# Optimization experiments

Hardware: AMD Instinct MI355X
Metric: run time of the kernel (lower is better)

Reference implementation:

```python
import jax, jax.numpy as jnp
import numpy as np

K = 20      # self.k in OurModel
TAU = 1.0   # self.tau in OurModel


def _knn_feats(emb, idx, yctx):
    # emb: [N, E] embedding table; idx: [B] int query ids; yctx: [B, N] residual context
    a = emb[idx]                                            # [B, E] gathered query embeddings
    # squared euclidean via gram trick, then sqrt == torch.cdist(p=2)
    d2 = (jnp.sum(a * a, axis=-1, keepdims=True)
          + jnp.sum(emb * emb, axis=-1)[None, :]
          - 2.0 * a @ emb.T)                                 # [B, N]
    sim = jnp.sqrt(jnp.clip(d2, 0.0, None)) + 0.001
    rows = jnp.arange(idx.shape[0])
    sim = sim.at[rows, idx].set(0.0)                         # zero self-distance
    w = jnp.exp(-sim / TAU)                                  # [B, N], self weight == 1 (max)
    # top (K+1) weights; drop the largest (the self entry) -> top-K neighbours.
    # Matches torch argsort(w)[:, -(K+1):-1]; downstream ops are order-invariant reductions.
    topw, topi = jax.lax.top_k(w, K + 1)
    topw = topw[:, 1:]                                       # [B, K]
    sel = jnp.take_along_axis(yctx, topi[:, 1:], axis=1)     # [B, K]
    f1 = jnp.sum(topw, axis=1)                               # sum of weights
    f2 = jnp.sum(sel * topw, axis=1) / jnp.sum(topw, axis=1) # weighted mean
    f3 = jnp.std(sel, axis=1, ddof=1)                        # torch.std is unbiased
    return f1, f2, f3


def _forward(emb0, emb1, rctx0, rctx1, idx0, idx1, mean_in, std_in,
             W1, b1, Wm, bm, Ws, bs):
    a1, a2, a3 = _knn_feats(emb0, idx0, rctx0)
    b1_, b2_, b3_ = _knn_feats(emb1, idx1, rctx1)
    # torch.cat(final1 + final2 + final3 + [mean, std]) column order
    feats = jnp.stack([a1, b1_, a2, b2_, a3, b3_, mean_in, std_in], axis=1)  # [B, 8]
    h = jnp.maximum(feats @ W1 + b1, 0.0)                    # [B, 64]
    mean_out = h @ Wm + bm[0]                                # [B]
    std_out = h @ Ws + bs[0]                                 # [B]
    return mean_out, std_out


def setup_inputs() -> dict:
    key = jax.random.key(0)
    ks = jax.random.split(key, 14)
    B, N, E, H = 512, 50000, 16, 64
    return {
        "emb0": jax.random.normal(ks[0], (N, E), jnp.float32),
        "emb1": jax.random.normal(ks[1], (N, E), jnp.float32),
        "rctx0": jax.random.normal(ks[2], (B, N), jnp.float32),
        "rctx1": jax.random.normal(ks[3], (B, N), jnp.float32),
        "idx0": jax.random.randint(ks[4], (B,), 0, N, jnp.int32),
        "idx1": jax.random.randint(ks[5], (B,), 0, N, jnp.int32),
        "mean_in": jax.random.normal(ks[6], (B,), jnp.float32),
        "std_in": jax.random.normal(ks[7], (B,), jnp.float32),
        "W1": jax.random.normal(ks[8], (8, H), jnp.float32) * 0.1,
        "b1": jax.random.normal(ks[9], (H,), jnp.float32) * 0.1,
        "Wm": jax.random.normal(ks[10], (H,), jnp.float32) * 0.1,
        "bm": jax.random.normal(ks[11], (1,), jnp.float32) * 0.1,
        "Ws": jax.random.normal(ks[12], (H,), jnp.float32) * 0.1,
        "bs": jax.random.normal(ks[13], (1,), jnp.float32) * 0.1,
    }


def reference(emb0, emb1, rctx0, rctx1, idx0, idx1, mean_in, std_in,
              W1, b1, Wm, bm, Ws, bs):
    return _forward(emb0, emb1, rctx0, rctx1, idx0, idx1, mean_in, std_in,
                    W1, b1, Wm, bm, Ws, bs)
```

## Files before the change

### kernel.cpp

```cpp
#include <hip/hip_runtime.h>
#include <math.h>

typedef unsigned long long u64;
typedef unsigned int u32;
#define INF64 0xFFFFFFFFFFFFFFFFULL
#define FBIG 3.3e38f
#define KSEL 20
#define QT   32
#define CNK  32
#define CNKSH 5
#define CAP  256
#define PREFT 2
#define DEPS 0.5f
#define NTHR 512

typedef __bf16 bf16x8 __attribute__((ext_vector_type(8)));
typedef float  f32x16 __attribute__((ext_vector_type(16)));
typedef unsigned int uint4e __attribute__((ext_vector_type(4)));

static __device__ __forceinline__ u32 asu(float f) { return __builtin_bit_cast(u32, f); }
static __device__ __forceinline__ float trunchi(u32 u) { return __builtin_bit_cast(float, u & 0xffff0000u); }
#define PERM2(a,b) __builtin_amdgcn_perm((a),(b),0x07060302u)
static __device__ __forceinline__ bf16x8 mk8(u32 a, u32 b, u32 c, u32 d) {
    uint4e t = {a, b, c, d};
    return __builtin_bit_cast(bf16x8, t);
}
static __device__ __forceinline__ f32x16 zero16() {
    f32x16 z = {0.f,0.f,0.f,0.f,0.f,0.f,0.f,0.f,0.f,0.f,0.f,0.f,0.f,0.f,0.f,0.f};
    return z;
}

static __device__ __forceinline__ float dot16(
    float4 a0, float4 a1, float4 a2, float4 a3,
    float4 b0, float4 b1, float4 b2, float4 b3)
{
    float d = 0.f;
    d = fmaf(a0.x, b0.x, d); d = fmaf(a0.y, b0.y, d);
    d = fmaf(a0.z, b0.z, d); d = fmaf(a0.w, b0.w, d);
    d = fmaf(a1.x, b1.x, d); d = fmaf(a1.y, b1.y, d);
    d = fmaf(a1.z, b1.z, d); d = fmaf(a1.w, b1.w, d);
    d = fmaf(a2.x, b2.x, d); d = fmaf(a2.y, b2.y, d);
    d = fmaf(a2.z, b2.z, d); d = fmaf(a2.w, b2.w, d);
    d = fmaf(a3.x, b3.x, d); d = fmaf(a3.y, b3.y, d);
    d = fmaf(a3.z, b3.z, d); d = fmaf(a3.w, b3.w, d);
    return d;
}

static __device__ __forceinline__ void cvt_hilo(float4 f0, float4 f1, bf16x8& hi, bf16x8& lo) {
    u32 u0=asu(f0.x),u1=asu(f0.y),u2=asu(f0.z),u3=asu(f0.w);
    u32 u4=asu(f1.x),u5=asu(f1.y),u6=asu(f1.z),u7=asu(f1.w);
    hi = mk8(PERM2(u1,u0), PERM2(u3,u2), PERM2(u5,u4), PERM2(u7,u6));
    u32 w0=asu(f0.x-trunchi(u0)), w1=asu(f0.y-trunchi(u1));
    u32 w2=asu(f0.z-trunchi(u2)), w3=asu(f0.w-trunchi(u3));
    u32 w4=asu(f1.x-trunchi(u4)), w5=asu(f1.y-trunchi(u5));
    u32 w6=asu(f1.z-trunchi(u6)), w7=asu(f1.w-trunchi(u7));
    lo = mk8(PERM2(w1,w0), PERM2(w3,w2), PERM2(w5,w4), PERM2(w7,w6));
}

static __device__ __forceinline__ f32x16 tile_qe(
    const float* __restrict__ embS, int base, int col, int kb, int N,
    bf16x8 B1, bf16x8 B2)
{
    int row = base + col;
    row = min(row, N - 1);
    const float4* ep = (const float4*)(embS + (size_t)row * 16 + kb * 8);
    float4 f0 = ep[0], f1 = ep[1];
    bf16x8 A1, A2;
    cvt_hilo(f0, f1, A1, A2);
    f32x16 acc = zero16();
    acc = __builtin_amdgcn_mfma_f32_32x32x16_bf16(A1, B1, acc, 0, 0, 0);
    acc = __builtin_amdgcn_mfma_f32_32x32x16_bf16(A1, B2, acc, 0, 0, 0);
    acc = __builtin_amdgcn_mfma_f32_32x32x16_bf16(A2, B1, acc, 0, 0, 0);
    return acc;
}

__global__ __launch_bounds__(256) void norm_kernel(
    const float* __restrict__ emb0, const float* __restrict__ emb1,
    float* __restrict__ neBuf, int N, int npad)
{
    const int j = blockIdx.x * 256 + threadIdx.x;
    const float* __restrict__ e = blockIdx.y ? emb1 : emb0;
    float* __restrict__ o = neBuf + (size_t)blockIdx.y * npad;
    float v = FBIG;
    if (j < N) {
        const float4* p = (const float4*)(e + (size_t)j * 16);
        float4 e0=p[0],e1=p[1],e2=p[2],e3=p[3];
        v = dot16(e0,e1,e2,e3, e0,e1,e2,e3);
    }
    if (j < npad) o[j] = v;
}

__device__ __attribute__((noinline)) float bound21(const float* sMinq, int lane) {
    const u32 vb = (lane < 32) ? asu(sMinq[lane]) : 0xFFFFFFFFu;
    u32 T = 0;
#pragma unroll 1
    for (int bb = 30; bb >= 16; --bb) {
        u32 U = T | ((1u << bb) - 1u);
        int nle = __popcll(__ballot(vb <= U));
        if (nle < KSEL + 1) T |= (1u << bb);
    }
    return __uint_as_float(T | 0xFFFFu) + DEPS;
}

__device__ __attribute__((noinline)) void refine_q(
    const float* __restrict__ embS, const float* __restrict__ neS,
    const u32* __restrict__ sbufq, const float4* qp, float naq,
    int M, u64* __restrict__ dst, int lane)
{
    const float4 q0 = qp[0], q1 = qp[1], q2 = qp[2], q3 = qp[3];
    auto rk = [&](int i) -> u64 {
        int j = (int)sbufq[i];
        const float4* p = (const float4*)(embS + (size_t)j * 16);
        float4 e0 = p[0], e1 = p[1], e2 = p[2], e3 = p[3];
        float qe = dot16(q0, q1, q2, q3, e0, e1, e2, e3);
        float dd = fmaxf(fmaf(qe, -2.f, naq + neS[j]), 0.f);
        return ((u64)asu(dd) << 32) | (u32)j;
    };
    u64 k0 = (lane < M) ? rk(lane) : INF64;
    if (M <= 64) {
        u64 T = 0;
#pragma unroll 1
        for (int bb = 62; bb >= 32; --bb) {
            u64 U = T | ((1ull << bb) - 1ull);
            int nle = __popcll(__ballot(k0 <= U));
            if (nle < KSEL) T |= (1ull << bb);
        }
        {
            u64 U = T | 0xFFFFull;
            int m = __popcll(__ballot(k0 <= U));
            if (m == KSEL) T = U;
            else {
#pragma unroll 1
                for (int bb = 15; bb >= 0; --bb) {
                    u64 U2 = T | ((1ull << bb) - 1ull);
                    int nle = __popcll(__ballot(k0 <= U2));
                    if (nle < KSEL) T |= (1ull << bb);
                }
            }
        }
        u64 mm = __ballot(k0 <= T);
        if (k0 <= T) {
            int sl = __popcll(mm & ((1ull << lane) - 1ull));
            if (sl < KSEL) dst[sl] = k0;
        }
        for (int sl = __popcll(mm) + lane; sl < KSEL; sl += 64) dst[sl] = INF64;
    } else {
        u64 k1 = (lane + 64 < M)  ? rk(lane + 64)  : INF64;
        u64 k2 = (lane + 128 < M) ? rk(lane + 128) : INF64;
        u64 k3 = (lane + 192 < M) ? rk(lane + 192) : INF64;
        u64 T = 0;
#pragma unroll 1
        for (int bb = 62; bb >= 32; --bb) {
            u64 U = T | ((1ull << bb) - 1ull);
            int nle = __popcll(__ballot(k0 <= U)) + __popcll(__ballot(k1 <= U))
                    + __popcll(__ballot(k2 <= U)) + __popcll(__ballot(k3 <= U));
            if (nle < KSEL) T |= (1ull << bb);
        }
        {
            u64 U = T | 0xFFFFull;
            int m = __popcll(__ballot(k0 <= U)) + __popcll(__ballot(k1 <= U))
                  + __popcll(__ballot(k2 <= U)) + __popcll(__ballot(k3 <= U));
            if (m == KSEL) T = U;
            else {
#pragma unroll 1
                for (int bb = 15; bb >= 0; --bb) {
                    u64 U2 = T | ((1ull << bb) - 1ull);
                    int nle = __popcll(__ballot(k0 <= U2)) + __popcll(__ballot(k1 <= U2))
                            + __popcll(__ballot(k2 <= U2)) + __popcll(__ballot(k3 <= U2));
                    if (nle < KSEL) T |= (1ull << bb);
                }
            }
        }
        int basec = 0;
        {
            u64 mm = __ballot(k0 <= T);
            if (k0 <= T) { int sl = basec + __popcll(mm & ((1ull << lane) - 1ull)); if (sl < KSEL) dst[sl] = k0; }
            basec += __popcll(mm);
        }
        {
            u64 mm = __ballot(k1 <= T);
            if (k1 <= T) { int sl = basec + __popcll(mm & ((1ull << lane) - 1ull)); if (sl < KSEL) dst[sl] = k1; }
            basec += __popcll(mm);
        }
        {
            u64 mm = __ballot(k2 <= T);
            if (k2 <= T) { int sl = basec + __popcll(mm & ((1ull << lane) - 1ull)); if (sl < KSEL) dst[sl] = k2; }
            basec += __popcll(mm);
        }
        {
            u64 mm = __ballot(k3 <= T);
            if (k3 <= T) { int sl = basec + __popcll(mm & ((1ull << lane) - 1ull)); if (sl < KSEL) dst[sl] = k3; }
            basec += __popcll(mm);
        }
        for (int sl = basec + lane; sl < KSEL; sl += 64) dst[sl] = INF64;
    }
}

__global__ __launch_bounds__(NTHR, 8) void knn_scan_kernel(
    const float* __restrict__ emb0, const float* __restrict__ emb1,
    const int* __restrict__ idx0, const int* __restrict__ idx1,
    const float* __restrict__ neBuf,
    u64* __restrict__ chunkTop, int N, int B, int chlen)
{
    const int tid  = threadIdx.x;
    const int lane = tid & 63;
    const int wv   = tid >> 6;
    const int col  = lane & 31;
    const int kb   = lane >> 5;
    const int bx   = blockIdx.x;
    const int xcd  = bx & 7;
    const int s    = xcd & 1;
    const int t_   = (bx >> 3) * 4 + (xcd >> 1);
    const int c    = t_ & (CNK - 1);
    const int qt   = t_ >> CNKSH;
    const int qbase = qt * QT;
    const int jbeg = c * chlen;
    const int tpc  = chlen >> 5;
    const int npad = chlen * CNK;

    const float* __restrict__ embS = s ? emb1 : emb0;
    const int*   __restrict__ idxp = s ? idx1 : idx0;
    const float* __restrict__ neS  = neBuf + (size_t)s * npad;

    __shared__ float Qs[QT][16];
    __shared__ float naS[QT];
    __shared__ int   sq[QT];
    __shared__ int   scnt[QT];
    __shared__ float sthr[QT];
    __shared__ float sMin[QT][33];
    __shared__ u32   sbuf[QT][CAP];

    if (tid < QT) { sq[tid] = idxp[qbase + tid]; scnt[tid] = 0; }
    __syncthreads();
    if (tid < 128) {
        int q = tid >> 2, part = tid & 3;
        ((float4*)(&Qs[q][0]))[part] = ((const float4*)(embS + (size_t)sq[q] * 16))[part];
    }
    __syncthreads();
    if (tid < QT) {
        const float4* qp = (const float4*)(&Qs[tid][0]);
        float4 a0=qp[0],a1=qp[1],a2=qp[2],a3=qp[3];
        naS[tid] = dot16(a0,a1,a2,a3, a0,a1,a2,a3);
    }
    bf16x8 B1, B2;
    {
        const float4* qp = (const float4*)(&Qs[col][kb * 8]);
        float4 f0 = qp[0], f1 = qp[1];
        cvt_hilo(f0, f1, B1, B2);
    }
    __syncthreads();

    const float na_l  = naS[col];
    const int   self_l = sq[col];

    float m0v = FBIG, m1v = FBIG;
#define PINS(r, nef) { float v_ = fmaf(acc[r], -2.f, na_l + (nef)); \
    float t1_ = fminf(m1v, fmaxf(m0v, v_)); m0v = fminf(m0v, v_); m1v = t1_; }
    for (int pt = 0; pt < PREFT; ++pt) {
        const int t = wv + pt * 8;
        const int base = jbeg + t * 32;
        const float4* np_ = (const float4*)(neS + base + kb * 4);
        float4 n0 = np_[0], n1 = np_[2], n2 = np_[4], n3 = np_[6];
        f32x16 acc = tile_qe(embS, base, col, kb, N, B1, B2);
        PINS(0,n0.x)  PINS(1,n0.y)  PINS(2,n0.z)  PINS(3,n0.w)
        PINS(4,n1.x)  PINS(5,n1.y)  PINS(6,n1.z)  PINS(7,n1.w)
        PINS(8,n2.x)  PINS(9,n2.y)  PINS(10,n2.z) PINS(11,n2.w)
        PINS(12,n3.x) PINS(13,n3.y) PINS(14,n3.z) PINS(15,n3.w)
    }
#undef PINS
    sMin[col][(wv * 2 + kb) * 2 + 0] = fmaxf(m0v, 0.f);
    sMin[col][(wv * 2 + kb) * 2 + 1] = fmaxf(m1v, 0.f);
    __syncthreads();

    for (int qq = 0; qq < 4; ++qq) {
        const int q = wv * 4 + qq;
        float thr = bound21(&sMin[q][0], lane);
        if (lane == 0) sthr[q] = thr;
    }
    __syncthreads();
    const float thr_l = sthr[col];

#define EPI(r, nef) { float ad_ = fmaf(acc[r], -2.f, na_l + (nef)); \
    if (ad_ <= thr_l) msk |= (1u << (r)); }
    for (int t = wv; t < tpc; t += 8) {
        const int base = jbeg + t * 32;
        const float4* np_ = (const float4*)(neS + base + kb * 4);
        float4 n0 = np_[0], n1 = np_[2], n2 = np_[4], n3 = np_[6];
        f32x16 acc = tile_qe(embS, base, col, kb, N, B1, B2);
        u32 msk = 0;
        EPI(0,n0.x)  EPI(1,n0.y)  EPI(2,n0.z)  EPI(3,n0.w)
        EPI(4,n1.x)  EPI(5,n1.y)  EPI(6,n1.z)  EPI(7,n1.w)
        EPI(8,n2.x)  EPI(9,n2.y)  EPI(10,n2.z) EPI(11,n2.w)
        EPI(12,n3.x) EPI(13,n3.y) EPI(14,n3.z) EPI(15,n3.w)
        while (msk) {
            int r = __ffs(msk) - 1;
            msk &= msk - 1;
            int j = base + (r & 3) + 8 * (r >> 2) + 4 * kb;
            if (j != self_l) {
                int sl = atomicAdd(&scnt[col], 1);
                if (sl < CAP) sbuf[col][sl] = (u32)j;
            }
        }
    }
#undef EPI
    __syncthreads();

    for (int qq = 0; qq < 4; ++qq) {
        const int q = wv * 4 + qq;
        u64* dst = chunkTop + ((size_t)(s * B + qbase + q) * CNK + c) * KSEL;
        refine_q(embS, neS, &sbuf[q][0], (const float4*)(&Qs[q][0]), naS[q],
                 min(scnt[q], CAP), dst, lane);
    }
}

__global__ __launch_bounds__(128) void merge_mlp_kernel(
    const u64* __restrict__ chunkTop,
    const float* __restrict__ rctx0, const float* __restrict__ rctx1,
    const float* __restrict__ mean_in, const float* __restrict__ std_in,
    const float* __restrict__ W1, const float* __restrict__ b1,
    const float* __restrict__ Wm, const float* __restrict__ bm,
    const float* __restrict__ Ws, const float* __restrict__ bs,
    float* __restrict__ out, int N, int B)
{
    const int b = blockIdx.x;
    const int tid = threadIdx.x;
    const int s = tid >> 6;
    const int lane = tid & 63;
    __shared__ float sf[8];

    const u64* src = chunkTop + ((size_t)(s * B + b)) * (CNK * KSEL);
    u64 v0 = src[lane];
    u64 v1 = src[lane + 64];
    u64 v2 = src[lane + 128];
    u64 v3 = src[lane + 192];
    u64 v4 = src[lane + 256];
    u64 v5 = src[lane + 320];
    u64 v6 = src[lane + 384];
    u64 v7 = src[lane + 448];
    u64 v8 = src[lane + 512];
    u64 v9 = src[lane + 576];
#define NLE(U) (__popcll(__ballot(v0 <= (U))) + __popcll(__ballot(v1 <= (U))) \
              + __popcll(__ballot(v2 <= (U))) + __popcll(__ballot(v3 <= (U))) \
              + __popcll(__ballot(v4 <= (U))) + __popcll(__ballot(v5 <= (U))) \
              + __popcll(__ballot(v6 <= (U))) + __popcll(__ballot(v7 <= (U))) \
              + __popcll(__ballot(v8 <= (U))) + __popcll(__ballot(v9 <= (U))))
    u64 T = 0;
#pragma unroll 1
    for (int bb = 62; bb >= 32; --bb) {
        u64 U = T | ((1ull << bb) - 1ull);
        int nle = NLE(U);
        if (nle < KSEL) T |= (1ull << bb);
    }
    {
        u64 U = T | 0xFFFFull;
        int m = NLE(U);
        if (m == KSEL) T = U;
        else {
#pragma unroll 1
            for (int bb = 15; bb >= 0; --bb) {
                u64 U2 = T | ((1ull << bb) - 1ull);
                int nle = NLE(U2);
                if (nle < KSEL) T |= (1ull << bb);
            }
        }
    }
#undef NLE
    const float* __restrict__ rctx = s ? rctx1 : rctx0;
    float sw = 0.f, ssw = 0.f, ss = 0.f, ss2 = 0.f;
#define ACC(vx) if ((vx) <= T) { \
        float d2 = __uint_as_float((u32)((vx) >> 32)); \
        int j = (int)(u32)((vx) & 0xFFFFFFFFULL); \
        float sim = sqrtf(d2) + 0.001f; \
        float wr = expf(-sim); \
        float svr = rctx[(size_t)b * N + j]; \
        sw += wr; ssw += svr * wr; ss += svr; ss2 += svr * svr; }
    ACC(v0) ACC(v1) ACC(v2) ACC(v3) ACC(v4)
    ACC(v5) ACC(v6) ACC(v7) ACC(v8) ACC(v9)
#undef ACC
#pragma unroll
    for (int o = 32; o; o >>= 1) {
        sw  += __shfl_down(sw,  o, 64);
        ssw += __shfl_down(ssw, o, 64);
        ss  += __shfl_down(ss,  o, 64);
        ss2 += __shfl_down(ss2, o, 64);
    }
    if (lane == 0) {
        sf[0 + s] = sw;
        sf[2 + s] = ssw / sw;
        float mean = ss * (1.f / KSEL);
        float var = (ss2 - (float)KSEL * mean * mean) * (1.f / (KSEL - 1));
        sf[4 + s] = sqrtf(fmaxf(var, 0.f));
        if (s == 0) { sf[6] = mean_in[b]; sf[7] = std_in[b]; }
    }
    __syncthreads();

    if (tid < 64) {
        float f0 = sf[0], f1 = sf[1], f2 = sf[2], f3 = sf[3];
        float f4 = sf[4], f5 = sf[5], f6 = sf[6], f7 = sf[7];
        float h = b1[lane];
        h = fmaf(f0, W1[0 * 64 + lane], h);
        h = fmaf(f1, W1[1 * 64 + lane], h);
        h = fmaf(f2, W1[2 * 64 + lane], h);
        h = fmaf(f3, W1[3 * 64 + lane], h);
        h = fmaf(f4, W1[4 * 64 + lane], h);
        h = fmaf(f5, W1[5 * 64 + lane], h);
        h = fmaf(f6, W1[6 * 64 + lane], h);
        h = fmaf(f7, W1[7 * 64 + lane], h);
        h = fmaxf(h, 0.f);
        float mo = h * Wm[lane], so = h * Ws[lane];
#pragma unroll
        for (int o = 32; o; o >>= 1) {
            mo += __shfl_down(mo, o, 64);
            so += __shfl_down(so, o, 64);
        }
        if (lane == 0) {
            out[b] = mo + bm[0];
            out[B + b] = so + bs[0];
        }
    }
}

extern "C" void kernel_launch(void* const* d_in, const int* in_sizes, int n_in,
                              void* d_out, int out_size, void* d_ws, size_t ws_size,
                              hipStream_t stream) {
    const float* emb0    = (const float*)d_in[0];
    const float* emb1    = (const float*)d_in[1];
    const float* rctx0   = (const float*)d_in[2];
    const float* rctx1   = (const float*)d_in[3];
    const int*   idx0    = (const int*)d_in[4];
    const int*   idx1    = (const int*)d_in[5];
    const float* mean_in = (const float*)d_in[6];
    const float* std_in  = (const float*)d_in[7];
    const float* W1      = (const float*)d_in[8];
    const float* b1      = (const float*)d_in[9];
    const float* Wm      = (const float*)d_in[10];
    const float* bm      = (const float*)d_in[11];
    const float* Ws      = (const float*)d_in[12];
    const float* bs      = (const float*)d_in[13];

    const int B = in_sizes[4];
    const int N = in_sizes[0] / 16;

    int chlen = (((N + CNK - 1) / CNK) + 31) & ~31;
    int npad  = chlen * CNK;

    float* neBuf = (float*)d_ws;
    u64* chunkTop = (u64*)((char*)d_ws + (size_t)2 * npad * sizeof(float));

    norm_kernel<<<dim3(npad / 256, 2), 256, 0, stream>>>(emb0, emb1, neBuf, N, npad);

    knn_scan_kernel<<<dim3(2 * (B / QT) * CNK), NTHR, 0, stream>>>(
        emb0, emb1, idx0, idx1, neBuf, chunkTop, N, B, chlen);

    merge_mlp_kernel<<<dim3(B), 128, 0, stream>>>(
        chunkTop, rctx0, rctx1, mean_in, std_in,
        W1, b1, Wm, bm, Ws, bs, (float*)d_out, N, B);
}
```

Measured before the change: 281.6 us.

## Prepack bf16 hi/lo embeddings, fold norms into MFMA accumulator, quantize refine selection

A prep kernel now converts each embedding row once into packed bf16 hi/lo halves alongside the squared norms. The scan kernel loads these packed words directly instead of converting per tile. It also seeds the MFMA accumulator with -0.5*(|q|^2+|e|^2), so the epilogue becomes a single compare against a scaled threshold. The refine step ranks candidates by a 16-bit quantized distance key, falls back to full 64-bit keys only for ties, and the prefetch tile count is doubled. The cost is extra workspace and memory traffic for the packed copy, plus an extra tie-resolution path.

After: 289.0 us. 2.6% more time.

```diff
diff --git a/kernel.cpp b/kernel.cpp
--- a/kernel.cpp
+++ b/kernel.cpp
@@ -10,7 +10,7 @@
 #define CNK  32
 #define CNKSH 5
 #define CAP  256
-#define PREFT 2
+#define PREFT 4
 #define DEPS 0.5f
 #define NTHR 512
 
@@ -24,10 +24,6 @@
 static __device__ __forceinline__ bf16x8 mk8(u32 a, u32 b, u32 c, u32 d) {
     uint4e t = {a, b, c, d};
     return __builtin_bit_cast(bf16x8, t);
-}
-static __device__ __forceinline__ f32x16 zero16() {
-    f32x16 z = {0.f,0.f,0.f,0.f,0.f,0.f,0.f,0.f,0.f,0.f,0.f,0.f,0.f,0.f,0.f,0.f};
-    return z;
 }
 
 static __device__ __forceinline__ float dot16(
@@ -58,36 +54,46 @@
 }
 
 static __device__ __forceinline__ f32x16 tile_qe(
-    const float* __restrict__ embS, int base, int col, int kb, int N,
-    bf16x8 B1, bf16x8 B2)
+    const u32* __restrict__ packS, int base, int col, int kb, int N,
+    bf16x8 B1, bf16x8 B2, f32x16 acc)
 {
     int row = base + col;
     row = min(row, N - 1);
-    const float4* ep = (const float4*)(embS + (size_t)row * 16 + kb * 8);
-    float4 f0 = ep[0], f1 = ep[1];
-    bf16x8 A1, A2;
-    cvt_hilo(f0, f1, A1, A2);
-    f32x16 acc = zero16();
+    const uint4e* ph = (const uint4e*)(packS + (size_t)row * 16);
+    bf16x8 A1 = __builtin_bit_cast(bf16x8, ph[kb]);
+    bf16x8 A2 = __builtin_bit_cast(bf16x8, ph[2 + kb]);
     acc = __builtin_amdgcn_mfma_f32_32x32x16_bf16(A1, B1, acc, 0, 0, 0);
     acc = __builtin_amdgcn_mfma_f32_32x32x16_bf16(A1, B2, acc, 0, 0, 0);
     acc = __builtin_amdgcn_mfma_f32_32x32x16_bf16(A2, B1, acc, 0, 0, 0);
     return acc;
 }
 
-__global__ __launch_bounds__(256) void norm_kernel(
+__global__ __launch_bounds__(256) void prep_kernel(
     const float* __restrict__ emb0, const float* __restrict__ emb1,
-    float* __restrict__ neBuf, int N, int npad)
+    float* __restrict__ neBuf, u32* __restrict__ pack, int N, int npad)
 {
     const int j = blockIdx.x * 256 + threadIdx.x;
+    if (j >= npad) return;
     const float* __restrict__ e = blockIdx.y ? emb1 : emb0;
     float* __restrict__ o = neBuf + (size_t)blockIdx.y * npad;
+    uint4e* __restrict__ pk = (uint4e*)(pack + ((size_t)blockIdx.y * npad + j) * 16);
     float v = FBIG;
+    uint4e z = {0u, 0u, 0u, 0u};
+    uint4e s0 = z, s1 = z, s2 = z, s3 = z;
     if (j < N) {
         const float4* p = (const float4*)(e + (size_t)j * 16);
         float4 e0=p[0],e1=p[1],e2=p[2],e3=p[3];
         v = dot16(e0,e1,e2,e3, e0,e1,e2,e3);
-    }
-    if (j < npad) o[j] = v;
+        bf16x8 h0, l0, h1, l1;
+        cvt_hilo(e0, e1, h0, l0);
+        cvt_hilo(e2, e3, h1, l1);
+        s0 = __builtin_bit_cast(uint4e, h0);
+        s1 = __builtin_bit_cast(uint4e, h1);
+        s2 = __builtin_bit_cast(uint4e, l0);
+        s3 = __builtin_bit_cast(uint4e, l1);
+    }
+    o[j] = v;
+    pk[0] = s0; pk[1] = s1; pk[2] = s2; pk[3] = s3;
 }
 
 __device__ __attribute__((noinline)) float bound21(const float* sMinq, int lane) {
@@ -104,92 +110,109 @@
 
 __device__ __attribute__((noinline)) void refine_q(
     const float* __restrict__ embS, const float* __restrict__ neS,
-    const u32* __restrict__ sbufq, const float4* qp, float naq,
+    const u32* __restrict__ sbufq, const float4* qp, float naq, float thrq,
     int M, u64* __restrict__ dst, int lane)
 {
     const float4 q0 = qp[0], q1 = qp[1], q2 = qp[2], q3 = qp[3];
-    auto rk = [&](int i) -> u64 {
+    const float qsc = 65536.0f / (thrq + 0.25f);
+    auto rk = [&](int i, u32& di) -> u64 {
         int j = (int)sbufq[i];
         const float4* p = (const float4*)(embS + (size_t)j * 16);
         float4 e0 = p[0], e1 = p[1], e2 = p[2], e3 = p[3];
         float qe = dot16(q0, q1, q2, q3, e0, e1, e2, e3);
         float dd = fmaxf(fmaf(qe, -2.f, naq + neS[j]), 0.f);
+        di = min((u32)(dd * qsc), 0xFFFFu);
         return ((u64)asu(dd) << 32) | (u32)j;
     };
-    u64 k0 = (lane < M) ? rk(lane) : INF64;
     if (M <= 64) {
-        u64 T = 0;
-#pragma unroll 1
-        for (int bb = 62; bb >= 32; --bb) {
-            u64 U = T | ((1ull << bb) - 1ull);
-            int nle = __popcll(__ballot(k0 <= U));
-            if (nle < KSEL) T |= (1ull << bb);
-        }
-        {
-            u64 U = T | 0xFFFFull;
-            int m = __popcll(__ballot(k0 <= U));
-            if (m == KSEL) T = U;
-            else {
-#pragma unroll 1
-                for (int bb = 15; bb >= 0; --bb) {
-                    u64 U2 = T | ((1ull << bb) - 1ull);
-                    int nle = __popcll(__ballot(k0 <= U2));
-                    if (nle < KSEL) T |= (1ull << bb);
-                }
+        u32 d0 = 0xFFFFFFFFu; u64 k0 = INF64;
+        if (lane < M) k0 = rk(lane, d0);
+        u32 T = 0;
+#pragma unroll 1
+        for (int bb = 15; bb >= 0; --bb) {
+            u32 U = T | ((1u << bb) - 1u);
+            int nle = __popcll(__ballot(d0 <= U));
+            if (nle < KSEL) T |= (1u << bb);
+        }
+        int c1 = __popcll(__ballot(d0 < T));
+        int need = KSEL - c1;
+        bool sel;
+        if (__popcll(__ballot(d0 == T)) == need) {
+            sel = (d0 <= T);
+        } else {
+            u64 tk = (d0 == T) ? k0 : INF64;
+            u64 Tt = 0;
+#pragma unroll 1
+            for (int bb = 62; bb >= 0; --bb) {
+                u64 U = Tt | ((1ull << bb) - 1ull);
+                int nle = __popcll(__ballot(tk <= U));
+                if (nle < need) Tt |= (1ull << bb);
             }
-        }
-        u64 mm = __ballot(k0 <= T);
-        if (k0 <= T) {
-            int sl = __popcll(mm & ((1ull << lane) - 1ull));
-            if (sl < KSEL) dst[sl] = k0;
-        }
+            sel = (d0 < T) || ((d0 == T) && (tk <= Tt));
+        }
+        u64 mm = __ballot(sel);
+        if (sel) { int sl = __popcll(mm & ((1ull << lane) - 1ull)); if (sl < KSEL) dst[sl] = k0; }
         for (int sl = __popcll(mm) + lane; sl < KSEL; sl += 64) dst[sl] = INF64;
     } else {
-        u64 k1 = (lane + 64 < M)  ? rk(lane + 64)  : INF64;
-        u64 k2 = (lane + 128 < M) ? rk(lane + 128) : INF64;
-        u64 k3 = (lane + 192 < M) ? rk(lane + 192) : INF64;
-        u64 T = 0;
-#pragma unroll 1
-        for (int bb = 62; bb >= 32; --bb) {
-            u64 U = T | ((1ull << bb) - 1ull);
-            int nle = __popcll(__ballot(k0 <= U)) + __popcll(__ballot(k1 <= U))
-                    + __popcll(__ballot(k2 <= U)) + __popcll(__ballot(k3 <= U));
-            if (nle < KSEL) T |= (1ull << bb);
-        }
-        {
-            u64 U = T | 0xFFFFull;
-            int m = __popcll(__ballot(k0 <= U)) + __popcll(__ballot(k1 <= U))
-                  + __popcll(__ballot(k2 <= U)) + __popcll(__ballot(k3 <= U));
-            if (m == KSEL) T = U;
-            else {
-#pragma unroll 1
-                for (int bb = 15; bb >= 0; --bb) {
-                    u64 U2 = T | ((1ull << bb) - 1ull);
-                    int nle = __popcll(__ballot(k0 <= U2)) + __popcll(__ballot(k1 <= U2))
-                            + __popcll(__ballot(k2 <= U2)) + __popcll(__ballot(k3 <= U2));
-                    if (nle < KSEL) T |= (1ull << bb);
-                }
+        u32 d0=0xFFFFFFFFu, d1=0xFFFFFFFFu, d2_=0xFFFFFFFFu, d3=0xFFFFFFFFu;
+        u64 k0=INF64, k1=INF64, k2=INF64, k3=INF64;
+        if (lane < M)       k0 = rk(lane, d0);
+        if (lane + 64 < M)  k1 = rk(lane + 64, d1);
+        if (lane + 128 < M) k2 = rk(lane + 128, d2_);
+        if (lane + 192 < M) k3 = rk(lane + 192, d3);
+        u32 T = 0;
+#pragma unroll 1
+        for (int bb = 15; bb >= 0; --bb) {
+            u32 U = T | ((1u << bb) - 1u);
+            int nle = __popcll(__ballot(d0 <= U)) + __popcll(__ballot(d1 <= U))
+                    + __popcll(__ballot(d2_ <= U)) + __popcll(__ballot(d3 <= U));
+            if (nle < KSEL) T |= (1u << bb);
+        }
+        int c1 = __popcll(__ballot(d0 < T)) + __popcll(__ballot(d1 < T))
+               + __popcll(__ballot(d2_ < T)) + __popcll(__ballot(d3 < T));
+        int need = KSEL - c1;
+        int nt = __popcll(__ballot(d0 == T)) + __popcll(__ballot(d1 == T))
+               + __popcll(__ballot(d2_ == T)) + __popcll(__ballot(d3 == T));
+        bool s0, s1, s2, s3;
+        if (nt == need) {
+            s0 = (d0 <= T); s1 = (d1 <= T); s2 = (d2_ <= T); s3 = (d3 <= T);
+        } else {
+            u64 t0 = (d0 == T) ? k0 : INF64;
+            u64 t1 = (d1 == T) ? k1 : INF64;
+            u64 t2 = (d2_ == T) ? k2 : INF64;
+            u64 t3 = (d3 == T) ? k3 : INF64;
+            u64 Tt = 0;
+#pragma unroll 1
+            for (int bb = 62; bb >= 0; --bb) {
+                u64 U = Tt | ((1ull << bb) - 1ull);
+                int nle = __popcll(__ballot(t0 <= U)) + __popcll(__ballot(t1 <= U))
+                        + __popcll(__ballot(t2 <= U)) + __popcll(__ballot(t3 <= U));
+                if (nle < need) Tt |= (1ull << bb);
             }
+            s0 = (d0 < T) || ((d0 == T) && (t0 <= Tt));
+            s1 = (d1 < T) || ((d1 == T) && (t1 <= Tt));
+            s2 = (d2_ < T) || ((d2_ == T) && (t2 <= Tt));
+            s3 = (d3 < T) || ((d3 == T) && (t3 <= Tt));
         }
         int basec = 0;
         {
-            u64 mm = __ballot(k0 <= T);
-            if (k0 <= T) { int sl = basec + __popcll(mm & ((1ull << lane) - 1ull)); if (sl < KSEL) dst[sl] = k0; }
+            u64 mm = __ballot(s0);
+            if (s0) { int sl = basec + __popcll(mm & ((1ull << lane) - 1ull)); if (sl < KSEL) dst[sl] = k0; }
             basec += __popcll(mm);
         }
         {
-            u64 mm = __ballot(k1 <= T);
-            if (k1 <= T) { int sl = basec + __popcll(mm & ((1ull << lane) - 1ull)); if (sl < KSEL) dst[sl] = k1; }
+            u64 mm = __ballot(s1);
+            if (s1) { int sl = basec + __popcll(mm & ((1ull << lane) - 1ull)); if (sl < KSEL) dst[sl] = k1; }
             basec += __popcll(mm);
         }
         {
-            u64 mm = __ballot(k2 <= T);
-            if (k2 <= T) { int sl = basec + __popcll(mm & ((1ull << lane) - 1ull)); if (sl < KSEL) dst[sl] = k2; }
+            u64 mm = __ballot(s2);
+            if (s2) { int sl = basec + __popcll(mm & ((1ull << lane) - 1ull)); if (sl < KSEL) dst[sl] = k2; }
             basec += __popcll(mm);
         }
         {
-            u64 mm = __ballot(k3 <= T);
-            if (k3 <= T) { int sl = basec + __popcll(mm & ((1ull << lane) - 1ull)); if (sl < KSEL) dst[sl] = k3; }
+            u64 mm = __ballot(s3);
+            if (s3) { int sl = basec + __popcll(mm & ((1ull << lane) - 1ull)); if (sl < KSEL) dst[sl] = k3; }
             basec += __popcll(mm);
         }
         for (int sl = basec + lane; sl < KSEL; sl += 64) dst[sl] = INF64;
@@ -199,7 +222,7 @@
 __global__ __launch_bounds__(NTHR, 8) void knn_scan_kernel(
     const float* __restrict__ emb0, const float* __restrict__ emb1,
     const int* __restrict__ idx0, const int* __restrict__ idx1,
-    const float* __restrict__ neBuf,
+    const float* __restrict__ neBuf, const u32* __restrict__ pack,
     u64* __restrict__ chunkTop, int N, int B, int chlen)
 {
     const int tid  = threadIdx.x;
@@ -221,6 +244,7 @@
     const float* __restrict__ embS = s ? emb1 : emb0;
     const int*   __restrict__ idxp = s ? idx1 : idx0;
     const float* __restrict__ neS  = neBuf + (size_t)s * npad;
+    const u32*   __restrict__ packS = pack + (size_t)s * npad * 16;
 
     __shared__ float Qs[QT][16];
     __shared__ float naS[QT];
@@ -251,25 +275,37 @@
     __syncthreads();
 
     const float na_l  = naS[col];
+    const float nah   = -0.5f * na_l;
     const int   self_l = sq[col];
 
-    float m0v = FBIG, m1v = FBIG;
-#define PINS(r, nef) { float v_ = fmaf(acc[r], -2.f, na_l + (nef)); \
-    float t1_ = fminf(m1v, fmaxf(m0v, v_)); m0v = fminf(m0v, v_); m1v = t1_; }
+#define AINIT() { \
+    acc[0]=fmaf(n0.x,-0.5f,nah);  acc[1]=fmaf(n0.y,-0.5f,nah); \
+    acc[2]=fmaf(n0.z,-0.5f,nah);  acc[3]=fmaf(n0.w,-0.5f,nah); \
+    acc[4]=fmaf(n1.x,-0.5f,nah);  acc[5]=fmaf(n1.y,-0.5f,nah); \
+    acc[6]=fmaf(n1.z,-0.5f,nah);  acc[7]=fmaf(n1.w,-0.5f,nah); \
+    acc[8]=fmaf(n2.x,-0.5f,nah);  acc[9]=fmaf(n2.y,-0.5f,nah); \
+    acc[10]=fmaf(n2.z,-0.5f,nah); acc[11]=fmaf(n2.w,-0.5f,nah); \
+    acc[12]=fmaf(n3.x,-0.5f,nah); acc[13]=fmaf(n3.y,-0.5f,nah); \
+    acc[14]=fmaf(n3.z,-0.5f,nah); acc[15]=fmaf(n3.w,-0.5f,nah); }
+
+    float m0v = -FBIG, m1v = -FBIG;
+#define PINS(r) { float a_ = acc[r]; \
+    float t1_ = fmaxf(m1v, fminf(m0v, a_)); m0v = fmaxf(m0v, a_); m1v = t1_; }
     for (int pt = 0; pt < PREFT; ++pt) {
         const int t = wv + pt * 8;
         const int base = jbeg + t * 32;
         const float4* np_ = (const float4*)(neS + base + kb * 4);
         float4 n0 = np_[0], n1 = np_[2], n2 = np_[4], n3 = np_[6];
-        f32x16 acc = tile_qe(embS, base, col, kb, N, B1, B2);
-        PINS(0,n0.x)  PINS(1,n0.y)  PINS(2,n0.z)  PINS(3,n0.w)
-        PINS(4,n1.x)  PINS(5,n1.y)  PINS(6,n1.z)  PINS(7,n1.w)
-        PINS(8,n2.x)  PINS(9,n2.y)  PINS(10,n2.z) PINS(11,n2.w)
-        PINS(12,n3.x) PINS(13,n3.y) PINS(14,n3.z) PINS(15,n3.w)
+        f32x16 acc; AINIT();
+        acc = tile_qe(packS, base, col, kb, N, B1, B2, acc);
+        PINS(0)  PINS(1)  PINS(2)  PINS(3)
+        PINS(4)  PINS(5)  PINS(6)  PINS(7)
+        PINS(8)  PINS(9)  PINS(10) PINS(11)
+        PINS(12) PINS(13) PINS(14) PINS(15)
     }
 #undef PINS
-    sMin[col][(wv * 2 + kb) * 2 + 0] = fmaxf(m0v, 0.f);
-    sMin[col][(wv * 2 + kb) * 2 + 1] = fmaxf(m1v, 0.f);
+    sMin[col][(wv * 2 + kb) * 2 + 0] = fmaxf(-2.f * m0v, 0.f);
+    sMin[col][(wv * 2 + kb) * 2 + 1] = fmaxf(-2.f * m1v, 0.f);
     __syncthreads();
 
     for (int qq = 0; qq < 4; ++qq) {
@@ -279,19 +315,20 @@
     }
     __syncthreads();
     const float thr_l = sthr[col];
-
-#define EPI(r, nef) { float ad_ = fmaf(acc[r], -2.f, na_l + (nef)); \
-    if (ad_ <= thr_l) msk |= (1u << (r)); }
+    const float mth   = -0.5f * thr_l;
+
+#define EPI(r) { if (acc[r] >= mth) msk |= (1u << (r)); }
     for (int t = wv; t < tpc; t += 8) {
         const int base = jbeg + t * 32;
         const float4* np_ = (const float4*)(neS + base + kb * 4);
         float4 n0 = np_[0], n1 = np_[2], n2 = np_[4], n3 = np_[6];
-        f32x16 acc = tile_qe(embS, base, col, kb, N, B1, B2);
+        f32x16 acc; AINIT();
+        acc = tile_qe(packS, base, col, kb, N, B1, B2, acc);
         u32 msk = 0;
-        EPI(0,n0.x)  EPI(1,n0.y)  EPI(2,n0.z)  EPI(3,n0.w)
-        EPI(4,n1.x)  EPI(5,n1.y)  EPI(6,n1.z)  EPI(7,n1.w)
-        EPI(8,n2.x)  EPI(9,n2.y)  EPI(10,n2.z) EPI(11,n2.w)
-        EPI(12,n3.x) EPI(13,n3.y) EPI(14,n3.z) EPI(15,n3.w)
+        EPI(0)  EPI(1)  EPI(2)  EPI(3)
+        EPI(4)  EPI(5)  EPI(6)  EPI(7)
+        EPI(8)  EPI(9)  EPI(10) EPI(11)
+        EPI(12) EPI(13) EPI(14) EPI(15)
         while (msk) {
             int r = __ffs(msk) - 1;
             msk &= msk - 1;
@@ -303,12 +340,13 @@
         }
     }
 #undef EPI
+#undef AINIT
     __syncthreads();
 
     for (int qq = 0; qq < 4; ++qq) {
         const int q = wv * 4 + qq;
         u64* dst = chunkTop + ((size_t)(s * B + qbase + q) * CNK + c) * KSEL;
-        refine_q(embS, neS, &sbuf[q][0], (const float4*)(&Qs[q][0]), naS[q],
+        refine_q(embS, neS, &sbuf[q][0], (const float4*)(&Qs[q][0]), naS[q], sthr[q],
                  min(scnt[q], CAP), dst, lane);
     }
 }
@@ -445,12 +483,14 @@
     int npad  = chlen * CNK;
 
     float* neBuf = (float*)d_ws;
-    u64* chunkTop = (u64*)((char*)d_ws + (size_t)2 * npad * sizeof(float));
-
-    norm_kernel<<<dim3(npad / 256, 2), 256, 0, stream>>>(emb0, emb1, neBuf, N, npad);
+    u32*   pack  = (u32*)((char*)d_ws + (size_t)2 * npad * sizeof(float));
+    u64* chunkTop = (u64*)((char*)d_ws + (size_t)2 * npad * (sizeof(float) + 64));
+
+    prep_kernel<<<dim3((npad + 255) / 256, 2), 256, 0, stream>>>(
+        emb0, emb1, neBuf, pack, N, npad);
 
     knn_scan_kernel<<<dim3(2 * (B / QT) * CNK), NTHR, 0, stream>>>(
-        emb0, emb1, idx0, idx1, neBuf, chunkTop, N, B, chlen);
+        emb0, emb1, idx0, idx1, neBuf, pack, chunkTop, N, B, chlen);
 
     merge_mlp_kernel<<<dim3(B), 128, 0, stream>>>(
         chunkTop, rctx0, rctx1, mean_in, std_in,
```
